# Kernel tuning notes

Measured on AMD Instinct MI355X. Metric: run time of the kernel, lower is better.

## Reference

```python
import jax, jax.numpy as jnp
import numpy as np

B, S, H = 1, 2048, 2048
NH, NKV, HD = 32, 4, 128
G = NH // NKV            # query groups per kv head
EPS = 1e-6
THETA = 1000000.0


def _rmsnorm(x, w):
    # per-head RMSNorm over last (head_dim) axis
    var = jnp.mean(jnp.square(x), axis=-1, keepdims=True)
    return x * jax.lax.rsqrt(var + EPS) * w


def _rotate_half(x):
    x1, x2 = jnp.split(x, 2, axis=-1)
    return jnp.concatenate([-x2, x1], axis=-1)


def _rope(x, cos, sin):
    # x: [B,S,h,HD], cos/sin: [S,HD]
    c = cos[None, :, None, :]
    s = sin[None, :, None, :]
    return x * c + _rotate_half(x) * s


def setup_inputs() -> dict:
    key = jax.random.key(0)
    ks = jax.random.split(key, 7)
    inv_freq = 1.0 / (THETA ** (jnp.arange(0, HD, 2, dtype=jnp.float32) / HD))
    freqs = jnp.outer(jnp.arange(S, dtype=jnp.float32), inv_freq)  # [S, HD/2]
    emb = jnp.concatenate([freqs, freqs], axis=-1)                 # [S, HD]
    std = 0.02
    return {
        "hidden_states": jax.random.normal(ks[0], (B, S, H), jnp.float32),
        "wq": jax.random.normal(ks[1], (H, NH * HD), jnp.float32) * std,
        "wk": jax.random.normal(ks[2], (H, NKV * HD), jnp.float32) * std,
        "wv": jax.random.normal(ks[3], (H, NKV * HD), jnp.float32) * std,
        "wo": jax.random.normal(ks[4], (NH * HD, H), jnp.float32) * std,
        "q_norm_w": jnp.ones((HD,), jnp.float32),
        "k_norm_w": jnp.ones((HD,), jnp.float32),
        "cos": jnp.cos(emb),
        "sin": jnp.sin(emb),
    }


def reference(hidden_states, wq, wk, wv, wo, q_norm_w, k_norm_w, cos, sin):
    b, s, _ = hidden_states.shape
    q = (hidden_states @ wq).reshape(b, s, NH, HD)
    k = (hidden_states @ wk).reshape(b, s, NKV, HD)
    v = (hidden_states @ wv).reshape(b, s, NKV, HD)
    # QK per-head RMSNorm, then interleaved RoPE (rotate-half form)
    q = _rope(_rmsnorm(q, q_norm_w), cos, sin)
    k = _rope(_rmsnorm(k, k_norm_w), cos, sin)
    # GQA: group Q heads per KV head instead of materializing repeated K/V
    qg = q.reshape(b, s, NKV, G, HD)
    scaling = HD ** -0.5
    scores = jnp.einsum('bqhgd,bkhd->bhgqk', qg, k) * scaling  # [B,NKV,G,S,S]
    causal = jnp.tril(jnp.ones((s, s), bool))
    scores = jnp.where(causal, scores, jnp.finfo(scores.dtype).min)
    p = jax.nn.softmax(scores, axis=-1)
    attn = jnp.einsum('bhgqk,bkhd->bqhgd', p, v).reshape(b, s, NH * HD)
    return attn @ wo
```

## Files before the change

### kernel.cpp

```cpp
#include <hip/hip_runtime.h>
#include <hip/hip_bf16.h>
#include <stdint.h>

#define SEQ 2048
#define HDIM 128
#define NHEADS 32
#define NKVH 4

typedef unsigned short u16;
typedef __bf16 bf16_t;
typedef bf16_t bf16x8 __attribute__((ext_vector_type(8)));
typedef float floatx4 __attribute__((ext_vector_type(4)));

__device__ __forceinline__ float bf2f(u16 u) {
  union { uint32_t i; float f; } v; v.i = ((uint32_t)u) << 16; return v.f;
}
__device__ __forceinline__ u16 f2bf(float f) {
  if (__builtin_isnan(f)) return 0;
  union { float f; uint32_t i; } v; v.f = f;
  uint32_t r = v.i + 0x7fffu + ((v.i >> 16) & 1u);
  return (u16)(r >> 16);
}
__device__ __forceinline__ float loadf_any(const void* p, size_t i, int isbf) {
  return isbf ? bf2f(((const u16*)p)[i]) : ((const float*)p)[i];
}

__device__ __forceinline__ void gload_lds16(const u16* g, u16* l) {
  __builtin_amdgcn_global_load_lds((__attribute__((address_space(1))) void*)g,
                                   (__attribute__((address_space(3))) void*)l,
                                   16, 0, 0);
}

__device__ __forceinline__ floatx4 mfma16(bf16x8 a, bf16x8 b, floatx4 c) {
  return __builtin_amdgcn_mfma_f32_16x16x32_bf16(a, b, c, 0, 0, 0);
}

struct InPack { const u16* p[9]; int n[9]; };

__global__ void detect_all(InPack pk, int* __restrict__ flags) {
  const int which = blockIdx.x;
  const u16* x = pk.p[which];
  const int n = pk.n[which];
  __shared__ int s_sane, s_zeven, s_zodd;
  if (threadIdx.x == 0) { s_sane = 0; s_zeven = 0; s_zodd = 0; }
  __syncthreads();
  const int ns = n < 8192 ? n : 8192;
  int sane = 0, zeven = 0, zodd = 0;
  for (int i = threadIdx.x; i < ns; i += 256) {
    const u16 u = x[i];
    const int e = (u >> 7) & 0xff;
    if ((e >= 96 && e <= 159) || u == 0) sane++;
    if (u == 0) { if (i & 1) zodd++; else zeven++; }
  }
#pragma unroll
  for (int off = 32; off >= 1; off >>= 1) {
    sane += __shfl_xor(sane, off, 64);
    zeven += __shfl_xor(zeven, off, 64);
    zodd += __shfl_xor(zodd, off, 64);
  }
  if ((threadIdx.x & 63) == 0) {
    atomicAdd(&s_sane, sane);
    atomicAdd(&s_zeven, zeven);
    atomicAdd(&s_zodd, zodd);
  }
  __syncthreads();
  if (threadIdx.x == 0) {
    const int even = (ns + 1) / 2, odd = ns / 2;
    const bool mostly_sane = (s_sane * 10 >= ns * 9);
    const bool fp32_const_pattern = (s_zeven * 2 >= even) && (s_zodd * 10 <= odd);
    flags[which] = (mostly_sane && !fp32_const_pattern) ? 1 : 0;
    if (which == 0) flags[15] = 1;
  }
}

__device__ __forceinline__ void transpose_tile(
    u16 (&tile)[64][65], const void* __restrict__ in, u16* __restrict__ out,
    int R, int C, int isbf, int bx, int by) {
  const int c0 = bx * 64, r0 = by * 64;
  const int t = threadIdx.x;
#pragma unroll
  for (int i = 0; i < 16; i++) {
    const int idx = i * 256 + t;
    const int r = idx >> 6, c = idx & 63;
    tile[r][c] = (u16)(isbf ? ((const u16*)in)[(size_t)(r0 + r) * C + c0 + c]
                            : f2bf(((const float*)in)[(size_t)(r0 + r) * C + c0 + c]));
  }
  __syncthreads();
#pragma unroll
  for (int i = 0; i < 16; i++) {
    const int idx = i * 256 + t;
    const int cc = idx >> 6, rr = idx & 63;
    out[(size_t)(c0 + cc) * R + r0 + rr] = tile[rr][cc];
  }
}

__global__ __launch_bounds__(256) void prep_all(
    const void* __restrict__ hs, const void* __restrict__ wq,
    const void* __restrict__ wk, const void* __restrict__ wv,
    u16* __restrict__ Hb, u16* __restrict__ wqkvT,
    const int* __restrict__ flags) {
  __shared__ u16 tile[64][65];
  const int b = blockIdx.x;
  if (b < 2048) {
    transpose_tile(tile, wq, wqkvT, 2048, 4096, flags[1], b & 63, b >> 6);
  } else if (b < 2304) {
    const int r = b - 2048;
    transpose_tile(tile, wk, wqkvT + 4096ull * 2048, 2048, 512, flags[2],
                   r & 7, r >> 3);
  } else if (b < 2560) {
    const int r = b - 2304;
    transpose_tile(tile, wv, wqkvT + 4608ull * 2048, 2048, 512, flags[3],
                   r & 7, r >> 3);
  } else {
    const int r = b - 2560;
    const int isbf = flags[0];
#pragma unroll
    for (int i = 0; i < 4; i++) {
      const int idx = (r * 4 + i) * 256 + threadIdx.x;
      Hb[idx] = isbf ? ((const u16*)hs)[idx] : f2bf(((const float*)hs)[idx]);
    }
  }
}

__global__ __launch_bounds__(256) void transpose_any(
    const void* __restrict__ in, u16* __restrict__ out, int R, int C,
    const int* __restrict__ flag) {
  __shared__ u16 tile[64][65];
  transpose_tile(tile, in, out, R, C, *flag, blockIdx.x, blockIdx.y);
}

__global__ __launch_bounds__(256) void gemm_bt_bf16(
    const u16* __restrict__ A, const u16* __restrict__ BT,
    void* __restrict__ C, int M, int N, int K,
    const int* __restrict__ cflag) {
  __shared__ alignas(16) u16 As[128 * 32];
  __shared__ alignas(16) u16 Bs[128 * 32];
  const int t = threadIdx.x;
  const int w = t >> 6;
  const int lane = t & 63;
  const int lhi = lane >> 4, llo = lane & 15;
  const int m0 = blockIdx.y * 128, n0 = blockIdx.x * 128;
  const int wm = (w & 1) * 64, wn = (w >> 1) * 64;

  floatx4 acc[4][4];
#pragma unroll
  for (int i = 0; i < 4; i++)
#pragma unroll
    for (int j = 0; j < 4; j++) acc[i][j] = (floatx4)(0.0f);

  for (int k0 = 0; k0 < K; k0 += 32) {
#pragma unroll
    for (int r = 0; r < 2; r++) {
      const int c = r * 256 + t;
      const int row = c >> 2, kc = c & 3;
      const int base = (r * 256 + w * 64) * 8;
      gload_lds16(A + (size_t)(m0 + row) * K + k0 + kc * 8, &As[base]);
      gload_lds16(BT + (size_t)(n0 + row) * K + k0 + kc * 8, &Bs[base]);
    }
    __syncthreads();
    bf16x8 af[4], bfr[4];
#pragma unroll
    for (int i = 0; i < 4; i++)
      af[i] = *(const bf16x8*)&As[(wm + i * 16 + llo) * 32 + lhi * 8];
#pragma unroll
    for (int j = 0; j < 4; j++)
      bfr[j] = *(const bf16x8*)&Bs[(wn + j * 16 + llo) * 32 + lhi * 8];
#pragma unroll
    for (int i = 0; i < 4; i++)
#pragma unroll
      for (int j = 0; j < 4; j++)
        acc[i][j] = mfma16(af[i], bfr[j], acc[i][j]);
    __syncthreads();
  }
  const int cbf = *cflag;
#pragma unroll
  for (int i = 0; i < 4; i++) {
    const int row0 = m0 + wm + i * 16 + lhi * 4;
#pragma unroll
    for (int j = 0; j < 4; j++) {
      const int col = n0 + wn + j * 16 + llo;
#pragma unroll
      for (int r = 0; r < 4; r++) {
        if (cbf) ((u16*)C)[(size_t)(row0 + r) * N + col] = f2bf(acc[i][j][r]);
        else ((float*)C)[(size_t)(row0 + r) * N + col] = acc[i][j][r];
      }
    }
  }
}

__global__ __launch_bounds__(1024) void gemm_bt_splitk(
    const u16* __restrict__ A, const u16* __restrict__ BT,
    void* __restrict__ C, int M, int N, int K,
    const int* __restrict__ cflag) {
  __shared__ alignas(16) u16 smem[4][2][128 * 32];
  const int t = threadIdx.x;
  const int g = t >> 8;
  const int tg = t & 255;
  const int w = tg >> 6;
  const int lane = t & 63;
  const int lhi = lane >> 4, llo = lane & 15;
  const int m0 = blockIdx.y * 128, n0 = blockIdx.x * 128;
  const int wm = (w & 1) * 64, wn = (w >> 1) * 64;
  const int kq = K >> 2;
  const int kbeg = g * kq;
  u16* As = smem[g][0];
  u16* Bs = smem[g][1];

  floatx4 acc[4][4];
#pragma unroll
  for (int i = 0; i < 4; i++)
#pragma unroll
    for (int j = 0; j < 4; j++) acc[i][j] = (floatx4)(0.0f);

  for (int k0 = 0; k0 < kq; k0 += 32) {
#pragma unroll
    for (int r = 0; r < 2; r++) {
      const int c = r * 256 + tg;
      const int row = c >> 2, kc = c & 3;
      const int base = (r * 256 + w * 64) * 8;
      gload_lds16(A + (size_t)(m0 + row) * K + kbeg + k0 + kc * 8, &As[base]);
      gload_lds16(BT + (size_t)(n0 + row) * K + kbeg + k0 + kc * 8, &Bs[base]);
    }
    __syncthreads();
    bf16x8 af[4], bfr[4];
#pragma unroll
    for (int i = 0; i < 4; i++)
      af[i] = *(const bf16x8*)&As[(wm + i * 16 + llo) * 32 + lhi * 8];
#pragma unroll
    for (int j = 0; j < 4; j++)
      bfr[j] = *(const bf16x8*)&Bs[(wn + j * 16 + llo) * 32 + lhi * 8];
#pragma unroll
    for (int i = 0; i < 4; i++)
#pragma unroll
      for (int j = 0; j < 4; j++)
        acc[i][j] = mfma16(af[i], bfr[j], acc[i][j]);
    __syncthreads();
  }

  float* red = (float*)&smem[0][0][0];
  for (int gg = 0; gg < 4; gg++) {
    if (g == gg) {
#pragma unroll
      for (int i = 0; i < 4; i++)
#pragma unroll
        for (int j = 0; j < 4; j++) {
          const int col = wn + j * 16 + llo;
#pragma unroll
          for (int r = 0; r < 4; r++) {
            const int row = wm + i * 16 + lhi * 4 + r;
            if (gg == 0) red[row * 128 + col] = acc[i][j][r];
            else red[row * 128 + col] += acc[i][j][r];
          }
        }
    }
    __syncthreads();
  }
  const int cbf = *cflag;
#pragma unroll
  for (int i = 0; i < 16; i++) {
    const int idx = i * 1024 + t;
    const int rr = idx >> 7, cc = idx & 127;
    const float v = red[rr * 128 + cc];
    if (cbf) ((u16*)C)[(size_t)(m0 + rr) * N + n0 + cc] = f2bf(v);
    else ((float*)C)[(size_t)(m0 + rr) * N + n0 + cc] = v;
  }
}

__global__ __launch_bounds__(128) void norm_rope_inplace(
    u16* __restrict__ QKV,
    const void* __restrict__ qw, const void* __restrict__ kw,
    const void* __restrict__ cosb, const void* __restrict__ sinb,
    const int* __restrict__ flags) {
  const int qwbf = flags[5], kwbf = flags[6], cbf = flags[7], sbf = flags[8];
  const int s = blockIdx.x, hy = blockIdx.y, d = threadIdx.x;
  const bool isQ = hy < NHEADS;
  const int col = isQ ? hy * HDIM : 4096 + (hy - NHEADS) * HDIM;
  u16* ptr = QKV + (size_t)s * 5120 + col + d;
  const float x = bf2f(*ptr);
  float v = x * x;
#pragma unroll
  for (int off = 32; off >= 1; off >>= 1) v += __shfl_xor(v, off, 64);
  __shared__ float sw[2];
  __shared__ float sh[128];
  if ((d & 63) == 0) sw[d >> 6] = v;
  __syncthreads();
  const float mean = (sw[0] + sw[1]) * (1.0f / 128.0f);
  const float rn = rsqrtf(mean + 1e-6f);
  const float wv = isQ ? loadf_any(qw, d, qwbf) : loadf_any(kw, d, kwbf);
  const float xn = x * rn * wv;
  sh[d] = xn;
  __syncthreads();
  const float other = sh[d ^ 64];
  const float cv = loadf_any(cosb, (size_t)s * HDIM + d, cbf);
  const float sv = loadf_any(sinb, (size_t)s * HDIM + d, sbf);
  const float o = xn * cv + (d < 64 ? -other : other) * sv;
  *ptr = f2bf(o);
}

__global__ __launch_bounds__(256) void v_transpose(
    const u16* __restrict__ QKV, u16* __restrict__ Vt) {
  __shared__ u16 tile[64][65];
  const int s0 = blockIdx.x * 64, d0 = blockIdx.y * 64, hk = blockIdx.z;
  const int t = threadIdx.x;
#pragma unroll
  for (int i = 0; i < 16; i++) {
    const int idx = i * 256 + t;
    const int r = idx >> 6, c = idx & 63;
    tile[r][c] = QKV[(size_t)(s0 + r) * 5120 + 4608 + hk * HDIM + d0 + c];
  }
  __syncthreads();
#pragma unroll
  for (int i = 0; i < 16; i++) {
    const int idx = i * 256 + t;
    const int dd = idx >> 6, ss = idx & 63;
    Vt[((size_t)hk * HDIM + d0 + dd) * SEQ + s0 + ss] = tile[ss][dd];
  }
}

__global__ __launch_bounds__(256) void flash_attn(
    const u16* __restrict__ QKV, const u16* __restrict__ Vt,
    u16* __restrict__ O) {
  __shared__ alignas(16) u16 Klds[64 * 128];
  __shared__ alignas(16) u16 Vlds[128 * 64];
  __shared__ alignas(16) u16 Plds[4][32 * 72];
  const int t = threadIdx.x;
  const int w = t >> 6;
  const int lane = t & 63;
  const int lhi = lane >> 4, llo = lane & 15;
  const int b = blockIdx.x;
  const int bi = b & 255;
  const int qt = (b < 256) ? (15 - (bi >> 5)) : (bi >> 5);
  const int h = bi & 31, hk = h >> 3;
  const int q0 = qt * 128;
  const int qw0 = q0 + w * 32;
  const float scale = 0.08838834764831845f;
  const float SMAX = 16.0f;

  bf16x8 qf[2][4];
#pragma unroll
  for (int i = 0; i < 2; i++)
#pragma unroll
    for (int c = 0; c < 4; c++)
      qf[i][c] = *(const bf16x8*)(QKV + (size_t)(qw0 + i * 16 + llo) * 5120 +
                                  h * HDIM + c * 32 + lhi * 8);

  floatx4 oacc[2][8];
  float lacc[2][4];
#pragma unroll
  for (int i = 0; i < 2; i++) {
#pragma unroll
    for (int d = 0; d < 8; d++) oacc[i][d] = (floatx4)(0.0f);
#pragma unroll
    for (int r = 0; r < 4; r++) lacc[i][r] = 0.0f;
  }

  const int ntiles = 2 * qt + 2;
  for (int tt = 0; tt < ntiles; tt++) {
    const int kv0 = tt * 64;
#pragma unroll
    for (int r = 0; r < 4; r++) {
      const int c = r * 256 + t;
      const int base = (r * 256 + w * 64) * 8;
      gload_lds16(QKV + (size_t)(kv0 + (c >> 4)) * 5120 + 4096 + hk * HDIM +
                      (((c & 15) ^ ((c >> 4) & 7)) * 8),
                  &Klds[base]);
      gload_lds16(Vt + ((size_t)hk * HDIM + (c >> 3)) * SEQ + kv0 +
                      (((c & 7) ^ ((c >> 3) & 7)) * 8),
                  &Vlds[base]);
    }
    __syncthreads();

    floatx4 sacc[2][4];
#pragma unroll
    for (int i = 0; i < 2; i++)
#pragma unroll
      for (int j = 0; j < 4; j++) sacc[i][j] = (floatx4)(0.0f);
#pragma unroll
    for (int j = 0; j < 4; j++) {
#pragma unroll
      for (int c = 0; c < 4; c++) {
        bf16x8 kf = *(const bf16x8*)&Klds[(j * 16 + llo) * 128 +
                                          (((c * 4 + lhi) ^ (llo & 7)) * 8)];
        sacc[0][j] = mfma16(qf[0][c], kf, sacc[0][j]);
        sacc[1][j] = mfma16(qf[1][c], kf, sacc[1][j]);
      }
    }
    if (kv0 + 64 > q0) {
#pragma unroll
      for (int i = 0; i < 2; i++)
#pragma unroll
        for (int j = 0; j < 4; j++) {
          const int n = kv0 + j * 16 + llo;
#pragma unroll
          for (int r = 0; r < 4; r++) {
            const int mm = qw0 + i * 16 + lhi * 4 + r;
            if (n > mm) sacc[i][j][r] = -30000.0f;
          }
        }
    }
#pragma unroll
    for (int i = 0; i < 2; i++)
#pragma unroll
      for (int j = 0; j < 4; j++)
#pragma unroll
        for (int r = 0; r < 4; r++) {
          const float p = __expf(fmaf(sacc[i][j][r], scale, -SMAX));
          lacc[i][r] += p;
          *(bf16_t*)&Plds[w][(i * 16 + lhi * 4 + r) * 72 + j * 16 + llo] =
              (bf16_t)p;
        }
    asm volatile("" ::: "memory");
    __builtin_amdgcn_s_waitcnt(0);
    asm volatile("" ::: "memory");
#pragma unroll
    for (int c = 0; c < 2; c++) {
      bf16x8 pf0 = *(const bf16x8*)&Plds[w][llo * 72 + c * 32 + lhi * 8];
      bf16x8 pf1 = *(const bf16x8*)&Plds[w][(16 + llo) * 72 + c * 32 + lhi * 8];
#pragma unroll
      for (int d = 0; d < 8; d++) {
        bf16x8 vf = *(const bf16x8*)&Vlds[(d * 16 + llo) * 64 +
                                          (((c * 4 + lhi) ^ (llo & 7)) * 8)];
        oacc[0][d] = mfma16(pf0, vf, oacc[0][d]);
        oacc[1][d] = mfma16(pf1, vf, oacc[1][d]);
      }
    }
    __syncthreads();
  }
#pragma unroll
  for (int i = 0; i < 2; i++)
#pragma unroll
    for (int r = 0; r < 4; r++) {
#pragma unroll
      for (int off = 1; off < 16; off <<= 1)
        lacc[i][r] += __shfl_xor(lacc[i][r], off, 64);
      const float linv = 1.0f / lacc[i][r];
      const int row = qw0 + i * 16 + lhi * 4 + r;
#pragma unroll
      for (int d = 0; d < 8; d++)
        O[(size_t)row * 4096 + h * HDIM + d * 16 + llo] =
            f2bf(oacc[i][d][r] * linv);
    }
}

extern "C" void kernel_launch(void* const* d_in, const int* in_sizes, int n_in,
                              void* d_out, int out_size, void* d_ws, size_t ws_size,
                              hipStream_t stream) {
  char* ws = (char*)d_ws;
  u16* wqkvT  = (u16*)(ws);
  u16* QKVp   = (u16*)(ws + (20ull << 20));
  u16* Vt     = (u16*)(ws + (40ull << 20));
  int* flags  = (int*)(ws + (42ull << 20));
  u16* attnO  = wqkvT;
  u16* woT    = QKVp;
  u16* Hb     = (u16*)d_out;

  InPack pk;
  for (int i = 0; i < 9; i++) { pk.p[i] = (const u16*)d_in[i]; pk.n[i] = in_sizes[i]; }
  detect_all<<<9, 256, 0, stream>>>(pk, flags);

  prep_all<<<6656, 256, 0, stream>>>(
      d_in[0], d_in[1], d_in[2], d_in[3], Hb, wqkvT, flags);

  gemm_bt_bf16<<<dim3(40, 16), 256, 0, stream>>>(
      Hb, wqkvT, QKVp, 2048, 5120, 2048, flags + 15);

  norm_rope_inplace<<<dim3(2048, NHEADS + NKVH), 128, 0, stream>>>(
      QKVp, d_in[5], d_in[6], d_in[7], d_in[8], flags);
  v_transpose<<<dim3(32, 2, 4), 256, 0, stream>>>(QKVp, Vt);

  flash_attn<<<512, 256, 0, stream>>>(QKVp, Vt, attnO);

  transpose_any<<<dim3(32, 64), 256, 0, stream>>>(d_in[4], woT, 4096, 2048, flags + 4);
  gemm_bt_splitk<<<dim3(16, 16), 1024, 0, stream>>>(
      attnO, woT, d_out, 2048, 2048, 4096, flags + 0);
}
```

Measured before the change: 401.5 us.

## Double-buffer K/V tiles in LDS and split P staging into halves

```diff
diff --git a/kernel.cpp b/kernel.cpp
--- a/kernel.cpp
+++ b/kernel.cpp
@@ -317,12 +317,95 @@
   }
 }
 
+__device__ __forceinline__ void fa_stage(
+    const u16* __restrict__ QKV, const u16* __restrict__ Vt,
+    u16* __restrict__ Kdst, u16* __restrict__ Vdst,
+    int kv0, int hk, int t, int w) {
+#pragma unroll
+  for (int r = 0; r < 4; r++) {
+    const int c = r * 256 + t;
+    const int base = (r * 256 + w * 64) * 8;
+    gload_lds16(QKV + (size_t)(kv0 + (c >> 4)) * 5120 + 4096 + hk * HDIM +
+                    (((c & 15) ^ ((c >> 4) & 7)) * 8),
+                &Kdst[base]);
+    gload_lds16(Vt + ((size_t)hk * HDIM + (c >> 3)) * SEQ + kv0 +
+                    (((c & 7) ^ ((c >> 3) & 7)) * 8),
+                &Vdst[base]);
+  }
+}
+
+__device__ __forceinline__ void fa_compute(
+    const u16* __restrict__ Kb, const u16* __restrict__ Vb,
+    u16* __restrict__ Pw, const bf16x8 (&qf)[2][4],
+    floatx4 (&oacc)[2][8], float (&lacc)[2][4],
+    int kv0, int q0, int qw0, int lhi, int llo) {
+  const float scale = 0.08838834764831845f;
+  const float SMAX = 16.0f;
+  floatx4 sacc[2][4];
+#pragma unroll
+  for (int i = 0; i < 2; i++)
+#pragma unroll
+    for (int j = 0; j < 4; j++) sacc[i][j] = (floatx4)(0.0f);
+#pragma unroll
+  for (int j = 0; j < 4; j++) {
+#pragma unroll
+    for (int c = 0; c < 4; c++) {
+      bf16x8 kf = *(const bf16x8*)&Kb[(j * 16 + llo) * 128 +
+                                      (((c * 4 + lhi) ^ (llo & 7)) * 8)];
+      sacc[0][j] = mfma16(qf[0][c], kf, sacc[0][j]);
+      sacc[1][j] = mfma16(qf[1][c], kf, sacc[1][j]);
+    }
+  }
+  if (kv0 + 64 > q0) {
+#pragma unroll
+    for (int i = 0; i < 2; i++)
+#pragma unroll
+      for (int j = 0; j < 4; j++) {
+        const int n = kv0 + j * 16 + llo;
+#pragma unroll
+        for (int r = 0; r < 4; r++) {
+          const int mm = qw0 + i * 16 + lhi * 4 + r;
+          if (n > mm) sacc[i][j][r] = -30000.0f;
+        }
+      }
+  }
+#pragma unroll
+  for (int hh = 0; hh < 2; hh++) {
+#pragma unroll
+    for (int i = 0; i < 2; i++)
+#pragma unroll
+      for (int jj = 0; jj < 2; jj++) {
+        const int j = hh * 2 + jj;
+#pragma unroll
+        for (int r = 0; r < 4; r++) {
+          const float p = __expf(fmaf(sacc[i][j][r], scale, -SMAX));
+          lacc[i][r] += p;
+          *(bf16_t*)&Pw[(i * 16 + lhi * 4 + r) * 40 + jj * 16 + llo] =
+              (bf16_t)p;
+        }
+      }
+    asm volatile("s_waitcnt lgkmcnt(0)" ::: "memory");
+    __builtin_amdgcn_sched_barrier(0);
+    bf16x8 pf0 = *(const bf16x8*)&Pw[llo * 40 + lhi * 8];
+    bf16x8 pf1 = *(const bf16x8*)&Pw[(16 + llo) * 40 + lhi * 8];
+#pragma unroll
+    for (int d = 0; d < 8; d++) {
+      bf16x8 vf = *(const bf16x8*)&Vb[(d * 16 + llo) * 64 +
+                                      (((hh * 4 + lhi) ^ (llo & 7)) * 8)];
+      oacc[0][d] = mfma16(pf0, vf, oacc[0][d]);
+      oacc[1][d] = mfma16(pf1, vf, oacc[1][d]);
+    }
+  }
+}
+
 __global__ __launch_bounds__(256) void flash_attn(
     const u16* __restrict__ QKV, const u16* __restrict__ Vt,
     u16* __restrict__ O) {
-  __shared__ alignas(16) u16 Klds[64 * 128];
-  __shared__ alignas(16) u16 Vlds[128 * 64];
-  __shared__ alignas(16) u16 Plds[4][32 * 72];
+  __shared__ alignas(16) u16 KldsA[64 * 128];
+  __shared__ alignas(16) u16 KldsB[64 * 128];
+  __shared__ alignas(16) u16 VldsA[128 * 64];
+  __shared__ alignas(16) u16 VldsB[128 * 64];
+  __shared__ alignas(16) u16 Plds[4][32 * 40];
   const int t = threadIdx.x;
   const int w = t >> 6;
   const int lane = t & 63;
@@ -333,8 +416,6 @@
   const int h = bi & 31, hk = h >> 3;
   const int q0 = qt * 128;
   const int qw0 = q0 + w * 32;
-  const float scale = 0.08838834764831845f;
-  const float SMAX = 16.0f;
 
   bf16x8 qf[2][4];
 #pragma unroll
@@ -355,76 +436,17 @@
   }
 
   const int ntiles = 2 * qt + 2;
-  for (int tt = 0; tt < ntiles; tt++) {
-    const int kv0 = tt * 64;
-#pragma unroll
-    for (int r = 0; r < 4; r++) {
-      const int c = r * 256 + t;
-      const int base = (r * 256 + w * 64) * 8;
-      gload_lds16(QKV + (size_t)(kv0 + (c >> 4)) * 5120 + 4096 + hk * HDIM +
-                      (((c & 15) ^ ((c >> 4) & 7)) * 8),
-                  &Klds[base]);
-      gload_lds16(Vt + ((size_t)hk * HDIM + (c >> 3)) * SEQ + kv0 +
-                      (((c & 7) ^ ((c >> 3) & 7)) * 8),
-                  &Vlds[base]);
-    }
-    __syncthreads();
-
-    floatx4 sacc[2][4];
-#pragma unroll
-    for (int i = 0; i < 2; i++)
-#pragma unroll
-      for (int j = 0; j < 4; j++) sacc[i][j] = (floatx4)(0.0f);
-#pragma unroll
-    for (int j = 0; j < 4; j++) {
-#pragma unroll
-      for (int c = 0; c < 4; c++) {
-        bf16x8 kf = *(const bf16x8*)&Klds[(j * 16 + llo) * 128 +
-                                          (((c * 4 + lhi) ^ (llo & 7)) * 8)];
-        sacc[0][j] = mfma16(qf[0][c], kf, sacc[0][j]);
-        sacc[1][j] = mfma16(qf[1][c], kf, sacc[1][j]);
-      }
-    }
-    if (kv0 + 64 > q0) {
-#pragma unroll
-      for (int i = 0; i < 2; i++)
-#pragma unroll
-        for (int j = 0; j < 4; j++) {
-          const int n = kv0 + j * 16 + llo;
-#pragma unroll
-          for (int r = 0; r < 4; r++) {
-            const int mm = qw0 + i * 16 + lhi * 4 + r;
-            if (n > mm) sacc[i][j][r] = -30000.0f;
-          }
-        }
-    }
-#pragma unroll
-    for (int i = 0; i < 2; i++)
-#pragma unroll
-      for (int j = 0; j < 4; j++)
-#pragma unroll
-        for (int r = 0; r < 4; r++) {
-          const float p = __expf(fmaf(sacc[i][j][r], scale, -SMAX));
-          lacc[i][r] += p;
-          *(bf16_t*)&Plds[w][(i * 16 + lhi * 4 + r) * 72 + j * 16 + llo] =
-              (bf16_t)p;
-        }
-    asm volatile("" ::: "memory");
-    __builtin_amdgcn_s_waitcnt(0);
-    asm volatile("" ::: "memory");
-#pragma unroll
-    for (int c = 0; c < 2; c++) {
-      bf16x8 pf0 = *(const bf16x8*)&Plds[w][llo * 72 + c * 32 + lhi * 8];
-      bf16x8 pf1 = *(const bf16x8*)&Plds[w][(16 + llo) * 72 + c * 32 + lhi * 8];
-#pragma unroll
-      for (int d = 0; d < 8; d++) {
-        bf16x8 vf = *(const bf16x8*)&Vlds[(d * 16 + llo) * 64 +
-                                          (((c * 4 + lhi) ^ (llo & 7)) * 8)];
-        oacc[0][d] = mfma16(pf0, vf, oacc[0][d]);
-        oacc[1][d] = mfma16(pf1, vf, oacc[1][d]);
-      }
-    }
-    __syncthreads();
+  fa_stage(QKV, Vt, KldsA, VldsA, 0, hk, t, w);
+  for (int tt = 0; tt < ntiles; tt += 2) {
+    __syncthreads();
+    fa_stage(QKV, Vt, KldsB, VldsB, (tt + 1) * 64, hk, t, w);
+    fa_compute(KldsA, VldsA, &Plds[w][0], qf, oacc, lacc,
+               tt * 64, q0, qw0, lhi, llo);
+    __syncthreads();
+    if (tt + 2 < ntiles)
+      fa_stage(QKV, Vt, KldsA, VldsA, (tt + 2) * 64, hk, t, w);
+    fa_compute(KldsB, VldsB, &Plds[w][0], qf, oacc, lacc,
+               (tt + 1) * 64, q0, qw0, lhi, llo);
   }
 #pragma unroll
   for (int i = 0; i < 2; i++)
```

Result: no change. 405.1 us (+0.9%).
